# Kernel tuning notes

Hardware: AMD Instinct MI355X
Metric: run time of the kernel (lower is better)

Reference implementation:

```python
import jax, jax.numpy as jnp
import numpy as np

N = 100000  # num nodes


def gcn_conv(x, edge_index, W, b):
    # PyG GCNConv (eval): x' = D^-1/2 (A + I) D^-1/2 (x @ W) + b
    x = x @ W  # [N, out]
    row = jnp.concatenate([edge_index[0], jnp.arange(N)])  # sources (+ self loops)
    col = jnp.concatenate([edge_index[1], jnp.arange(N)])  # targets (+ self loops)
    ones = jnp.ones(row.shape[0], dtype=x.dtype)
    deg = jax.ops.segment_sum(ones, col, num_segments=N)
    dis = jnp.where(deg > 0, jax.lax.rsqrt(jnp.maximum(deg, 1.0)), 0.0)
    norm = dis[row] * dis[col]  # [E+N]
    msg = norm[:, None] * x[row]  # gather + scale
    out = jax.ops.segment_sum(msg, col, num_segments=N)  # scatter-add
    return out + b


def setup_inputs() -> dict:
    key = jax.random.key(0)
    k1, k2, k3, k4 = jax.random.split(key, 4)
    F_in, H, F_out = 512, 16, 40
    x = jax.random.normal(k1, (N, F_in), dtype=jnp.float32)
    edge_index = jax.random.randint(k2, (2, 3200000), 0, N, dtype=jnp.int64)
    W1 = jax.random.normal(k3, (F_in, H), dtype=jnp.float32) / np.sqrt(F_in)
    b1 = jnp.zeros((H,), dtype=jnp.float32)
    W2 = jax.random.normal(k4, (H, F_out), dtype=jnp.float32) / np.sqrt(H)
    b2 = jnp.zeros((F_out,), dtype=jnp.float32)
    return {"x": x, "edge_index": edge_index, "W1": W1, "b1": b1, "W2": W2, "b2": b2}


def reference(x, edge_index, W1, b1, W2, b2):
    # eval mode: no drop_edge, no dropout
    h = jax.nn.relu(gcn_conv(x, edge_index, W1, b1))
    return gcn_conv(h, edge_index, W2, b2)
```

## Files before the change

kernel.cpp:

```cpp
#include <hip/hip_runtime.h>

#define F_IN 512
#define HDIM 16
#define F_OUT 40
#define BTGT 64
#define REPL 8
#define NCH 512
#define ECH 2048

typedef unsigned short ushortT;

__device__ __forceinline__ unsigned f2bf(float f) {
  unsigned u = __float_as_uint(f);
  u += 0x7FFF + ((u >> 16) & 1);
  return u >> 16;
}
__device__ __forceinline__ float bf2f(ushortT b) {
  return __uint_as_float(((unsigned)b) << 16);
}
__device__ __forceinline__ float bf2f_lo(unsigned w) {
  return __uint_as_float(w << 16);
}
__device__ __forceinline__ float bf2f_hi(unsigned w) {
  return __uint_as_float(w & 0xFFFF0000u);
}

__device__ __forceinline__ int load_src(const void* ei, int is64, int e) {
  return is64 ? (int)((const unsigned int*)ei)[2 * (long long)e] : ((const int*)ei)[e];
}
__device__ __forceinline__ int load_dst(const void* ei, int is64, int e, int E) {
  long long i = (long long)E + e;
  return is64 ? (int)((const unsigned int*)ei)[2 * i] : ((const int*)ei)[i];
}

extern "C" __global__ void k_init(int* __restrict__ hist, int m, int* __restrict__ flag) {
  int i = blockIdx.x * blockDim.x + threadIdx.x;
  if (i < m) hist[i] = 0;
  if (i == 0) *flag = 1;
}

extern "C" __global__ void k_detect(const unsigned int* __restrict__ w, int npairs,
                                    int* __restrict__ flag) {
  int i = blockIdx.x * blockDim.x + threadIdx.x;
  if (i < npairs && w[2 * i + 1] != 0u) atomicAnd(flag, 0);
}

extern "C" __global__ __launch_bounds__(256) void k_hist(const void* __restrict__ ei, int E,
                                                         int echunk, int* __restrict__ hist,
                                                         int NBK,
                                                         const int* __restrict__ flag) {
  extern __shared__ int lh[];
  int g = blockIdx.x, t = threadIdx.x;
  for (int i = t; i < NBK; i += 256) lh[i] = 0;
  __syncthreads();
  int is64 = *flag;
  int e0 = g * echunk;
  int e1 = e0 + echunk;
  if (e1 > E) e1 = E;
  if (e0 < e1) {
    if (is64 && ((E & 1) == 0)) {
      const int* w32 = (const int*)ei;
      int evend = e0 + ((e1 - e0) & ~1);
      for (int e = e0 + 2 * t; e + 1 < evend + 2; e += 512) {
        if (e + 1 >= e1) break;
        int4 d4 = *(const int4*)(w32 + 2 * ((size_t)E + e));
        atomicAdd(&lh[(unsigned)d4.x >> 6], 1);
        atomicAdd(&lh[(unsigned)d4.z >> 6], 1);
      }
      for (int e = evend + t; e < e1; e += 256)
        atomicAdd(&lh[(unsigned)load_dst(ei, 1, e, E) >> 6], 1);
    } else {
      for (int e = e0 + t; e < e1; e += 256)
        atomicAdd(&lh[(unsigned)load_dst(ei, is64, e, E) >> 6], 1);
    }
  }
  __syncthreads();
  int repl = g & (REPL - 1);
  for (int i = t; i < NBK; i += 256) {
    int v = lh[i];
    if (v) atomicAdd(&hist[i * REPL + repl], v);
  }
}

extern "C" __global__ __launch_bounds__(1024) void k_scanb(const int* __restrict__ hist,
                                                           int* __restrict__ boffs,
                                                           int* __restrict__ bcur, int M) {
  __shared__ int sh[1024];
  int tid = threadIdx.x;
  int C = (M + 1023) / 1024;
  int base = tid * C;
  int s = 0;
  for (int k = 0; k < C; k++) {
    int idx = base + k;
    if (idx < M) s += hist[idx];
  }
  sh[tid] = s;
  __syncthreads();
  for (int d = 1; d < 1024; d <<= 1) {
    int t2 = (tid >= d) ? sh[tid - d] : 0;
    __syncthreads();
    sh[tid] += t2;
    __syncthreads();
  }
  int run = sh[tid] - s;
  for (int k = 0; k < C; k++) {
    int idx = base + k;
    if (idx < M) {
      int v = hist[idx];
      boffs[idx] = run;
      bcur[idx] = run;
      run += v;
    }
  }
  if (tid == 1023) boffs[M] = run;
}

extern "C" __global__ __launch_bounds__(256) void k_bucket(const void* __restrict__ ei, int E,
                                                           int echunk, int* __restrict__ bcur,
                                                           unsigned int* __restrict__ bked,
                                                           const int* __restrict__ flag) {
  int g = blockIdx.x, t = threadIdx.x;
  int is64 = *flag;
  int repl = g & (REPL - 1);
  int e0 = g * echunk;
  int e1 = e0 + echunk;
  if (e1 > E) e1 = E;
  if (e0 >= e1) return;
  if (is64 && ((E & 1) == 0)) {
    const int* w32 = (const int*)ei;
    int evend = e0 + ((e1 - e0) & ~1);
    for (int e = e0 + 2 * t; e + 1 < evend + 2; e += 512) {
      if (e + 1 >= e1) break;
      int4 s4 = *(const int4*)(w32 + 2 * (size_t)e);
      int4 d4 = *(const int4*)(w32 + 2 * ((size_t)E + e));
      {
        int idx = ((unsigned)d4.x >> 6) * REPL + repl;
        int p = atomicAdd(&bcur[idx], 1);
        __builtin_nontemporal_store(
            (unsigned)s4.x | ((unsigned)(d4.x & (BTGT - 1)) << 20), &bked[p]);
      }
      {
        int idx = ((unsigned)d4.z >> 6) * REPL + repl;
        int p = atomicAdd(&bcur[idx], 1);
        __builtin_nontemporal_store(
            (unsigned)s4.z | ((unsigned)(d4.z & (BTGT - 1)) << 20), &bked[p]);
      }
    }
    for (int e = evend + t; e < e1; e += 256) {
      int r = load_src(ei, 1, e);
      int c = load_dst(ei, 1, e, E);
      int idx = ((unsigned)c >> 6) * REPL + repl;
      int p = atomicAdd(&bcur[idx], 1);
      __builtin_nontemporal_store(
          (unsigned)r | ((unsigned)(c & (BTGT - 1)) << 20), &bked[p]);
    }
  } else {
    for (int e = e0 + t; e < e1; e += 256) {
      int r = load_src(ei, is64, e);
      int c = load_dst(ei, is64, e, E);
      int idx = ((unsigned)c >> 6) * REPL + repl;
      int p = atomicAdd(&bcur[idx], 1);
      __builtin_nontemporal_store(
          (unsigned)r | ((unsigned)(c & (BTGT - 1)) << 20), &bked[p]);
    }
  }
}

extern "C" __global__ __launch_bounds__(256, 2) void k_degb(
    const unsigned int* __restrict__ bked, const int* __restrict__ boffs,
    float* __restrict__ dis, int n) {
  __shared__ int lc[BTGT];
  __shared__ unsigned ebd[ECH];
  int b = blockIdx.x, t = threadIdx.x;
  if (t < BTGT) lc[t] = 0;
  __syncthreads();
  int beg = boffs[b * REPL], end = boffs[(b + 1) * REPL];
  for (int cbeg = beg; cbeg < end; cbeg += ECH) {
    int len = end - cbeg;
    if (len > ECH) len = ECH;
    for (int i = t; i < len; i += 256) ebd[i] = bked[cbeg + i];
    __syncthreads();
    for (int i = t; i < len; i += 256) atomicAdd(&lc[ebd[i] >> 20], 1);
    __syncthreads();
  }
  if (t < BTGT) {
    int i = b * BTGT + t;
    if (i < n) dis[i] = rsqrtf((float)lc[t] + 1.0f);
  }
}

extern "C" __global__ __launch_bounds__(256) void k_mm1s(
    const float* __restrict__ x, const float* __restrict__ W1, const float* __restrict__ dis,
    ushortT* __restrict__ hs, int n) {
  __shared__ float xs[256 * 32];
  __shared__ float w1s[F_IN * HDIM];
  int t = threadIdx.x;
  int row0 = blockIdx.x * 256;
  {
    const float4* wg = (const float4*)W1;
    float4* wl = (float4*)w1s;
    for (int i = t; i < F_IN * HDIM / 4; i += 256) wl[i] = wg[i];
  }
  int r = row0 + t;
  bool active = (r < n);
  bool fullblk = (row0 + 255 < n);
  float acc[HDIM];
#pragma unroll
  for (int j = 0; j < HDIM; j++) acc[j] = 0.f;

  float4* xs4 = (float4*)xs;
  for (int kc = 0; kc < F_IN / 32; kc++) {
    __syncthreads();
    if (fullblk) {
#pragma unroll
      for (int it = 0; it < 8; it++) {
        int f = it * 256 + t;
        int r2 = f >> 3, fi = f & 7;
        float4 v = ((const float4*)(x + (size_t)(row0 + r2) * F_IN + kc * 32))[fi];
        xs4[r2 * 8 + (fi ^ (r2 & 7))] = v;
      }
    } else {
      for (int it = 0; it < 8; it++) {
        int f = it * 256 + t;
        int r2 = f >> 3, fi = f & 7;
        float4 v = make_float4(0.f, 0.f, 0.f, 0.f);
        if (row0 + r2 < n)
          v = ((const float4*)(x + (size_t)(row0 + r2) * F_IN + kc * 32))[fi];
        xs4[r2 * 8 + (fi ^ (r2 & 7))] = v;
      }
    }
    __syncthreads();
    if (active) {
#pragma unroll
      for (int i = 0; i < 8; i++) {
        int ii = i ^ (t & 7);
        float4 xv = xs4[t * 8 + ii];
        float xk[4] = {xv.x, xv.y, xv.z, xv.w};
        int kb = kc * 32 + i * 4;
#pragma unroll
        for (int kk = 0; kk < 4; kk++) {
          const float4* wr = (const float4*)(w1s + (size_t)(kb + kk) * HDIM);
#pragma unroll
          for (int q = 0; q < HDIM / 4; q++) {
            float4 wv = wr[q];
            acc[4 * q + 0] = fmaf(xk[kk], wv.x, acc[4 * q + 0]);
            acc[4 * q + 1] = fmaf(xk[kk], wv.y, acc[4 * q + 1]);
            acc[4 * q + 2] = fmaf(xk[kk], wv.z, acc[4 * q + 2]);
            acc[4 * q + 3] = fmaf(xk[kk], wv.w, acc[4 * q + 3]);
          }
        }
      }
    }
  }
  if (active) {
    float d = dis[r];
    unsigned wds[8];
#pragma unroll
    for (int q = 0; q < 8; q++) {
      unsigned lo = f2bf(d * acc[2 * q]);
      unsigned hi = f2bf(d * acc[2 * q + 1]);
      wds[q] = lo | (hi << 16);
    }
    uint4* o = (uint4*)(hs + (size_t)r * HDIM);
    o[0] = make_uint4(wds[0], wds[1], wds[2], wds[3]);
    o[1] = make_uint4(wds[4], wds[5], wds[6], wds[7]);
  }
}

__device__ __forceinline__ void agg_body(const ushortT* __restrict__ feat,
                                         const unsigned int* __restrict__ bked,
                                         unsigned* __restrict__ eb,
                                         float* __restrict__ acc, int beg, int end, int t) {
  int g = t >> 3, j2 = t & 7;
  for (int cbeg = beg; cbeg < end; cbeg += ECH) {
    int len = end - cbeg;
    if (len > ECH) len = ECH;
    for (int i = t; i < len; i += 256) eb[i] = bked[cbeg + i];
    __syncthreads();
    int nf = len >> 8;
    for (int s = 0; s < nf; s++) {
      int base = (s << 8) + (g << 3);
      unsigned u[8];
#pragma unroll
      for (int k = 0; k < 8; k++) u[k] = eb[base + k];
      unsigned w[8];
#pragma unroll
      for (int k = 0; k < 8; k++)
        w[k] = *(const unsigned*)(feat + ((size_t)(u[k] & 0xFFFFFu) << 4) + (j2 << 1));
#pragma unroll
      for (int k = 0; k < 8; k++) {
        int a = ((u[k] >> 20) << 4) + (j2 << 1);
        atomicAdd(&acc[a], bf2f_lo(w[k]));
        atomicAdd(&acc[a + 1], bf2f_hi(w[k]));
      }
    }
    for (int i = (nf << 8) + g; i < len; i += 32) {
      unsigned u = eb[i];
      unsigned w = *(const unsigned*)(feat + ((size_t)(u & 0xFFFFFu) << 4) + (j2 << 1));
      int a = ((u >> 20) << 4) + (j2 << 1);
      atomicAdd(&acc[a], bf2f_lo(w));
      atomicAdd(&acc[a + 1], bf2f_hi(w));
    }
    __syncthreads();
  }
}

extern "C" __global__ __launch_bounds__(256, 2) void k_agg1(
    const ushortT* __restrict__ hs, const unsigned int* __restrict__ bked,
    const int* __restrict__ boffs, const float* __restrict__ dis,
    const float* __restrict__ b1, ushortT* __restrict__ zs, int n) {
  __shared__ float acc[BTGT * HDIM];
  __shared__ unsigned eb[ECH];
  int b = blockIdx.x, t = threadIdx.x;
  for (int k = t; k < BTGT * HDIM; k += 256) acc[k] = 0.f;
  __syncthreads();
  int beg = boffs[b * REPL], end = boffs[(b + 1) * REPL];
  agg_body(hs, bked, eb, acc, beg, end, t);
  int g = t >> 4, j = t & 15;
  for (int il = g; il < BTGT; il += 16) {
    int i = b * BTGT + il;
    if (i < n) {
      float di = dis[i];
      float v = di * (acc[il * HDIM + j] + bf2f(hs[(size_t)i * HDIM + j])) + b1[j];
      v = fmaxf(v, 0.f);
      zs[(size_t)i * HDIM + j] = (ushortT)f2bf(di * v);
    }
  }
}

extern "C" __global__ __launch_bounds__(256, 2) void k_agg2f(
    const ushortT* __restrict__ zs, const unsigned int* __restrict__ bked,
    const int* __restrict__ boffs, const float* __restrict__ dis,
    const float* __restrict__ W2, const float* __restrict__ b2, float* __restrict__ out,
    int n) {
  __shared__ float acc[BTGT * HDIM];
  __shared__ unsigned eb[ECH];
  __shared__ float w2s[HDIM * F_OUT];
  __shared__ float b2s[F_OUT];
  int b = blockIdx.x, t = threadIdx.x;
  for (int k = t; k < BTGT * HDIM; k += 256) acc[k] = 0.f;
  for (int k = t; k < HDIM * F_OUT; k += 256) w2s[k] = W2[k];
  if (t < F_OUT) b2s[t] = b2[t];
  __syncthreads();
  int beg = boffs[b * REPL], end = boffs[(b + 1) * REPL];
  agg_body(zs, bked, eb, acc, beg, end, t);
  int g = t >> 4, j = t & 15;
  for (int il = g; il < BTGT; il += 16) {
    int i = b * BTGT + il;
    if (i < n) {
      float di = dis[i];
      acc[il * HDIM + j] = di * (acc[il * HDIM + j] + bf2f(zs[(size_t)i * HDIM + j]));
    }
  }
  __syncthreads();
  int il = t >> 2, qo = t & 3;
  int i = b * BTGT + il;
  if (i < n) {
    float tv[HDIM];
#pragma unroll
    for (int k = 0; k < HDIM; k++) tv[k] = acc[il * HDIM + k];
#pragma unroll
    for (int jj = 0; jj < 10; jj++) {
      int col = qo * 10 + jj;
      float s = b2s[col];
#pragma unroll
      for (int k = 0; k < HDIM; k++) s = fmaf(tv[k], w2s[k * F_OUT + col], s);
      out[(size_t)i * F_OUT + col] = s;
    }
  }
}

extern "C" void kernel_launch(void* const* d_in, const int* in_sizes, int n_in,
                              void* d_out, int out_size, void* d_ws, size_t ws_size,
                              hipStream_t stream) {
  const float* x = (const float*)d_in[0];
  const void* ei = d_in[1];
  const float* W1 = (const float*)d_in[2];
  const float* b1 = (const float*)d_in[3];
  const float* W2 = (const float*)d_in[4];
  const float* b2 = (const float*)d_in[5];
  float* out = (float*)d_out;

  const int n = in_sizes[0] / F_IN;
  const int E = in_sizes[1] / 2;
  const int NBK = (n + BTGT - 1) / BTGT;
  const int M = NBK * REPL;
  int echunk = (E + NCH - 1) / NCH;
  echunk = (echunk + 1) & ~1;

  char* w = (char*)d_ws;
  auto alloc = [&](size_t bytes) {
    char* p = w;
    w += (bytes + 255) & ~(size_t)255;
    return p;
  };
  int* flag = (int*)alloc(4);
  int* hist = (int*)alloc((size_t)M * 4);
  int* boffs = (int*)alloc((size_t)(M + 1) * 4);
  int* bcur = (int*)alloc((size_t)M * 4);
  float* dis = (float*)alloc((size_t)n * 4);
  unsigned int* bked = (unsigned int*)alloc((size_t)E * 4);
  ushortT* hs = (ushortT*)alloc((size_t)n * HDIM * 2);
  ushortT* zs = (ushortT*)alloc((size_t)n * HDIM * 2);

  dim3 B(256);
  hipLaunchKernelGGL(k_init, dim3((M + 255) / 256), B, 0, stream, hist, M, flag);
  int npairs = 4096;
  if (npairs > E) npairs = E;
  hipLaunchKernelGGL(k_detect, dim3((npairs + 255) / 256), B, 0, stream,
                     (const unsigned int*)ei, npairs, flag);
  hipLaunchKernelGGL(k_hist, dim3(NCH), B, (size_t)NBK * 4, stream, ei, E, echunk, hist, NBK,
                     flag);
  hipLaunchKernelGGL(k_scanb, dim3(1), dim3(1024), 0, stream, hist, boffs, bcur, M);
  hipLaunchKernelGGL(k_bucket, dim3(NCH), B, 0, stream, ei, E, echunk, bcur, bked, flag);
  hipLaunchKernelGGL(k_degb, dim3(NBK), B, 0, stream, bked, boffs, dis, n);
  hipLaunchKernelGGL(k_mm1s, dim3((n + 255) / 256), B, 0, stream, x, W1, dis, hs, n);
  hipLaunchKernelGGL(k_agg1, dim3(NBK), B, 0, stream, hs, bked, boffs, dis, b1, zs, n);
  hipLaunchKernelGGL(k_agg2f, dim3(NBK), B, 0, stream, zs, bked, boffs, dis, W2, b2, out, n);
}
```

Before: 969.9 us.

## Aggregate edges per thread with full-row vector gathers and skewed LDS accumulators

Restructures the aggregation so each thread handles a whole edge: it loads the packed edge word directly from global memory with nontemporal loads and gathers the full 16-feature bf16 row as two 16-byte loads, instead of staging edge chunks in LDS and splitting rows across 8 lanes. Shared accumulators are indexed with a per-target rotation to spread atomic bank conflicts, and the readers are updated to match. The degree kernel also drops LDS staging, and the occupancy hint in launch bounds is removed. This cuts LDS staging and barriers but issues 16 LDS atomics per edge per thread and relies on more memory-level parallelism per thread.

```diff
diff --git a/kernel.cpp b/kernel.cpp
--- a/kernel.cpp
+++ b/kernel.cpp
@@ -6,7 +6,6 @@
 #define BTGT 64
 #define REPL 8
 #define NCH 512
-#define ECH 2048
 
 typedef unsigned short ushortT;
 
@@ -166,23 +165,16 @@
   }
 }
 
-extern "C" __global__ __launch_bounds__(256, 2) void k_degb(
+extern "C" __global__ __launch_bounds__(256) void k_degb(
     const unsigned int* __restrict__ bked, const int* __restrict__ boffs,
     float* __restrict__ dis, int n) {
   __shared__ int lc[BTGT];
-  __shared__ unsigned ebd[ECH];
   int b = blockIdx.x, t = threadIdx.x;
   if (t < BTGT) lc[t] = 0;
   __syncthreads();
   int beg = boffs[b * REPL], end = boffs[(b + 1) * REPL];
-  for (int cbeg = beg; cbeg < end; cbeg += ECH) {
-    int len = end - cbeg;
-    if (len > ECH) len = ECH;
-    for (int i = t; i < len; i += 256) ebd[i] = bked[cbeg + i];
-    __syncthreads();
-    for (int i = t; i < len; i += 256) atomicAdd(&lc[ebd[i] >> 20], 1);
-    __syncthreads();
-  }
+  for (int p = beg + t; p < end; p += 256) atomicAdd(&lc[bked[p] >> 20], 1);
+  __syncthreads();
   if (t < BTGT) {
     int i = b * BTGT + t;
     if (i < n) dis[i] = rsqrtf((float)lc[t] + 1.0f);
@@ -267,74 +259,73 @@
   }
 }
 
+__device__ __forceinline__ void edge_accum(const ushortT* __restrict__ feat,
+                                           float* __restrict__ acc, unsigned u) {
+  unsigned src = u & 0xFFFFFu;
+  int lc = (int)(u >> 20);
+  int base = lc << 4;
+  const uint4* rp = (const uint4*)(feat + ((size_t)src << 4));
+  uint4 q0 = rp[0];
+  uint4 q1 = rp[1];
+  float f[16];
+  f[0] = bf2f_lo(q0.x);  f[1] = bf2f_hi(q0.x);
+  f[2] = bf2f_lo(q0.y);  f[3] = bf2f_hi(q0.y);
+  f[4] = bf2f_lo(q0.z);  f[5] = bf2f_hi(q0.z);
+  f[6] = bf2f_lo(q0.w);  f[7] = bf2f_hi(q0.w);
+  f[8] = bf2f_lo(q1.x);  f[9] = bf2f_hi(q1.x);
+  f[10] = bf2f_lo(q1.y); f[11] = bf2f_hi(q1.y);
+  f[12] = bf2f_lo(q1.z); f[13] = bf2f_hi(q1.z);
+  f[14] = bf2f_lo(q1.w); f[15] = bf2f_hi(q1.w);
+#pragma unroll
+  for (int j = 0; j < 16; j++) atomicAdd(&acc[base + ((j + lc) & 15)], f[j]);
+}
+
 __device__ __forceinline__ void agg_body(const ushortT* __restrict__ feat,
                                          const unsigned int* __restrict__ bked,
-                                         unsigned* __restrict__ eb,
                                          float* __restrict__ acc, int beg, int end, int t) {
-  int g = t >> 3, j2 = t & 7;
-  for (int cbeg = beg; cbeg < end; cbeg += ECH) {
-    int len = end - cbeg;
-    if (len > ECH) len = ECH;
-    for (int i = t; i < len; i += 256) eb[i] = bked[cbeg + i];
-    __syncthreads();
-    int nf = len >> 8;
-    for (int s = 0; s < nf; s++) {
-      int base = (s << 8) + (g << 3);
-      unsigned u[8];
-#pragma unroll
-      for (int k = 0; k < 8; k++) u[k] = eb[base + k];
-      unsigned w[8];
-#pragma unroll
-      for (int k = 0; k < 8; k++)
-        w[k] = *(const unsigned*)(feat + ((size_t)(u[k] & 0xFFFFFu) << 4) + (j2 << 1));
-#pragma unroll
-      for (int k = 0; k < 8; k++) {
-        int a = ((u[k] >> 20) << 4) + (j2 << 1);
-        atomicAdd(&acc[a], bf2f_lo(w[k]));
-        atomicAdd(&acc[a + 1], bf2f_hi(w[k]));
-      }
-    }
-    for (int i = (nf << 8) + g; i < len; i += 32) {
-      unsigned u = eb[i];
-      unsigned w = *(const unsigned*)(feat + ((size_t)(u & 0xFFFFFu) << 4) + (j2 << 1));
-      int a = ((u >> 20) << 4) + (j2 << 1);
-      atomicAdd(&acc[a], bf2f_lo(w));
-      atomicAdd(&acc[a + 1], bf2f_hi(w));
-    }
-    __syncthreads();
-  }
-}
-
-extern "C" __global__ __launch_bounds__(256, 2) void k_agg1(
+  int p = beg + t;
+  for (; p + 256 < end; p += 512) {
+    unsigned u0 = __builtin_nontemporal_load(&bked[p]);
+    unsigned u1 = __builtin_nontemporal_load(&bked[p + 256]);
+    edge_accum(feat, acc, u0);
+    edge_accum(feat, acc, u1);
+  }
+  if (p < end) {
+    unsigned u = __builtin_nontemporal_load(&bked[p]);
+    edge_accum(feat, acc, u);
+  }
+}
+
+extern "C" __global__ __launch_bounds__(256) void k_agg1(
     const ushortT* __restrict__ hs, const unsigned int* __restrict__ bked,
     const int* __restrict__ boffs, const float* __restrict__ dis,
     const float* __restrict__ b1, ushortT* __restrict__ zs, int n) {
   __shared__ float acc[BTGT * HDIM];
-  __shared__ unsigned eb[ECH];
   int b = blockIdx.x, t = threadIdx.x;
   for (int k = t; k < BTGT * HDIM; k += 256) acc[k] = 0.f;
   __syncthreads();
   int beg = boffs[b * REPL], end = boffs[(b + 1) * REPL];
-  agg_body(hs, bked, eb, acc, beg, end, t);
+  agg_body(hs, bked, acc, beg, end, t);
+  __syncthreads();
   int g = t >> 4, j = t & 15;
   for (int il = g; il < BTGT; il += 16) {
     int i = b * BTGT + il;
     if (i < n) {
       float di = dis[i];
-      float v = di * (acc[il * HDIM + j] + bf2f(hs[(size_t)i * HDIM + j])) + b1[j];
+      float a = acc[(il << 4) + ((j + il) & 15)];
+      float v = di * (a + bf2f(hs[(size_t)i * HDIM + j])) + b1[j];
       v = fmaxf(v, 0.f);
       zs[(size_t)i * HDIM + j] = (ushortT)f2bf(di * v);
     }
   }
 }
 
-extern "C" __global__ __launch_bounds__(256, 2) void k_agg2f(
+extern "C" __global__ __launch_bounds__(256) void k_agg2f(
     const ushortT* __restrict__ zs, const unsigned int* __restrict__ bked,
     const int* __restrict__ boffs, const float* __restrict__ dis,
     const float* __restrict__ W2, const float* __restrict__ b2, float* __restrict__ out,
     int n) {
   __shared__ float acc[BTGT * HDIM];
-  __shared__ unsigned eb[ECH];
   __shared__ float w2s[HDIM * F_OUT];
   __shared__ float b2s[F_OUT];
   int b = blockIdx.x, t = threadIdx.x;
@@ -343,13 +334,15 @@
   if (t < F_OUT) b2s[t] = b2[t];
   __syncthreads();
   int beg = boffs[b * REPL], end = boffs[(b + 1) * REPL];
-  agg_body(zs, bked, eb, acc, beg, end, t);
+  agg_body(zs, bked, acc, beg, end, t);
+  __syncthreads();
   int g = t >> 4, j = t & 15;
   for (int il = g; il < BTGT; il += 16) {
     int i = b * BTGT + il;
     if (i < n) {
       float di = dis[i];
-      acc[il * HDIM + j] = di * (acc[il * HDIM + j] + bf2f(zs[(size_t)i * HDIM + j]));
+      int s = (il << 4) + ((j + il) & 15);
+      acc[s] = di * (acc[s] + bf2f(zs[(size_t)i * HDIM + j]));
     }
   }
   __syncthreads();
@@ -358,7 +351,7 @@
   if (i < n) {
     float tv[HDIM];
 #pragma unroll
-    for (int k = 0; k < HDIM; k++) tv[k] = acc[il * HDIM + k];
+    for (int k = 0; k < HDIM; k++) tv[k] = acc[(il << 4) + ((k + il) & 15)];
 #pragma unroll
     for (int jj = 0; jj < 10; jj++) {
       int col = qo * 10 + jj;
```

Result: no change. 957.2 us (-1.3%).
